# Kernel optimization log

Measured on AMD Instinct MI355X. Metric: run time of the kernel, lower is better.

The kernel has to match this reference:

```python
import jax, jax.numpy as jnp
import numpy as np

N_T, N_Q = 32768, 4096
E_T, E_Q = 1048576, 131072
H = 128
VOCAB = 1001  # num_features + 1
NUM_LAYERS = 3


def _sage_conv(x, edge_index, Wl, bl, Wr):
    # PyG SAGEConv, aggr='mean': out = lin_l(mean_j x_j) + lin_r(x_i)
    src, dst = edge_index[0], edge_index[1]
    n = x.shape[0]
    agg = jax.ops.segment_sum(x[src], dst, num_segments=n)          # [n, H]
    cnt = jax.ops.segment_sum(jnp.ones((src.shape[0],), x.dtype), dst, num_segments=n)
    mean = agg / jnp.maximum(cnt, 1.0)[:, None]
    return mean @ Wl.T + bl + x @ Wr.T


def setup_inputs() -> dict:
    key = jax.random.key(0)
    ks = jax.random.split(key, 12)
    target_x = jax.random.randint(ks[0], (N_T,), 0, VOCAB, dtype=jnp.int64 if jax.config.jax_enable_x64 else jnp.int32)
    query_x = jax.random.randint(ks[1], (N_Q,), 0, VOCAB, dtype=target_x.dtype)
    target_edge_index = jax.random.randint(ks[2], (2, E_T), 0, N_T, dtype=target_x.dtype)
    query_edge_index = jax.random.randint(ks[3], (2, E_Q), 0, N_Q, dtype=target_x.dtype)
    mask = jax.random.bernoulli(ks[4], 0.5, (N_Q, N_T))
    emb = jax.random.normal(ks[5], (VOCAB, H), jnp.float32) * 0.02
    s = 1.0 / np.sqrt(H)
    Wl = jax.random.uniform(ks[6], (NUM_LAYERS, H, H), jnp.float32, -s, s)
    bl = jax.random.uniform(ks[7], (NUM_LAYERS, H), jnp.float32, -s, s)
    Wr = jax.random.uniform(ks[8], (NUM_LAYERS, H, H), jnp.float32, -s, s)
    return {"target_x": target_x, "query_x": query_x,
            "target_edge_index": target_edge_index, "query_edge_index": query_edge_index,
            "mask": mask, "emb": emb, "Wl": Wl, "bl": bl, "Wr": Wr}


def reference(target_x, query_x, target_edge_index, query_edge_index, mask, emb, Wl, bl, Wr):
    et = emb[target_x]  # [N_T, H]
    eq = emb[query_x]   # [N_Q, H]
    for i in range(NUM_LAYERS):
        et = jax.nn.elu(_sage_conv(et, target_edge_index, Wl[i], bl[i], Wr[i]))
        eq = jax.nn.elu(_sage_conv(eq, query_edge_index, Wl[i], bl[i], Wr[i]))
    fmask = mask.astype(jnp.float32)
    att = (eq @ et.T) * fmask / jnp.sqrt(jnp.float32(H)) + (-1e9) * (1.0 - fmask)
    att = jax.nn.softmax(att, axis=1)
    return att[None]  # [1, N_Q, N_T]
```

## Files before the change

### kernel.cpp

```cpp
#include <hip/hip_runtime.h>
#include <stdint.h>

#define N_T 32768
#define N_Q 4096
#define E_T 1048576
#define E_Q 131072
#define H   128
#define NL  3
#define VOCAB 1001

typedef float    f32x4 __attribute__((ext_vector_type(4)));
typedef int      i32x4 __attribute__((ext_vector_type(4)));
typedef unsigned u32x4 __attribute__((ext_vector_type(4)));
typedef _Float16 f16x8 __attribute__((ext_vector_type(8)));

__device__ __forceinline__ ushort f2h(float x){
  union{_Float16 h; ushort u;} c; c.h = (_Float16)x; return c.u;
}
__device__ __forceinline__ float h2f(unsigned u){
  union{ushort u; _Float16 h;} c; c.u = (ushort)u; return (float)c.h;
}

__global__ void zero_i32_k(int* p, int n){
  int i = blockIdx.x*blockDim.x + threadIdx.x;
  if(i<n) p[i]=0;
}
__global__ void zero_f32_k(float* p, int n){
  int i = blockIdx.x*blockDim.x + threadIdx.x;
  if(i<n) p[i]=0.f;
}

__global__ void detect_mask_k(const unsigned* m, int* flag){
  int t = threadIdx.x;
  int f = 0;
  for(int j=t;j<4096;j+=256){
    unsigned v = m[j];
    if(v > 1u) f |= (v & 0xFEFEFEFEu) ? 2 : 1;
  }
  if(f) atomicOr(flag, f);
}

__global__ void wcvt_k(const float* __restrict__ Wl, const float* __restrict__ Wr,
                       ushort* __restrict__ WH, ushort* __restrict__ WLo){
  int i = blockIdx.x*blockDim.x + threadIdx.x;
  if(i >= NL*128*64) return;
  int k  = (i & 63) * 4;
  int c  = (i >> 6) & 127;
  int l  = i >> 13;
  const float* src = (k < 128)
      ? &Wl[((size_t)l*128 + c)*128 + k]
      : &Wr[((size_t)l*128 + c)*128 + (k-128)];
  float4 v = *(const float4*)src;
  ushort4 h, lo;
  h.x = f2h(v.x); lo.x = f2h(v.x - h2f(h.x));
  h.y = f2h(v.y); lo.y = f2h(v.y - h2f(h.y));
  h.z = f2h(v.z); lo.z = f2h(v.z - h2f(h.z));
  h.w = f2h(v.w); lo.w = f2h(v.w - h2f(h.w));
  size_t off = ((size_t)l*128 + c)*256 + k;
  *(ushort4*)&WH[off]  = h;
  *(ushort4*)&WLo[off] = lo;
}

__global__ void ecvt_k(const float* __restrict__ e, ushort* __restrict__ o){
  int i = blockIdx.x*blockDim.x + threadIdx.x;
  if(i >= VOCAB*H/8) return;
  float4 v0 = ((const float4*)e)[(size_t)i*2];
  float4 v1 = ((const float4*)e)[(size_t)i*2 + 1];
  uint4 u;
  u.x = (unsigned)f2h(v0.x) | ((unsigned)f2h(v0.y)<<16);
  u.y = (unsigned)f2h(v0.z) | ((unsigned)f2h(v0.w)<<16);
  u.z = (unsigned)f2h(v1.x) | ((unsigned)f2h(v1.y)<<16);
  u.w = (unsigned)f2h(v1.z) | ((unsigned)f2h(v1.w)<<16);
  ((uint4*)o)[i] = u;
}

__global__ void count_k(const int* __restrict__ dst, int E, int* cnt){
  int i = blockIdx.x*blockDim.x + threadIdx.x;
  if(i<E) atomicAdd(&cnt[dst[i]], 1);
}

__global__ void scan_k(const int* __restrict__ cnt, int n, int* rp, int* pos){
  __shared__ int part[1024];
  int t = threadIdx.x;
  int chunk = (n + 1023) >> 10;
  int lo = t*chunk, hi = lo+chunk; if(hi>n) hi=n;
  int s = 0;
  for(int i=lo;i<hi;i++) s += cnt[i];
  part[t] = s;
  __syncthreads();
  for(int off=1; off<1024; off<<=1){
    int v = (t >= off) ? part[t-off] : 0;
    __syncthreads();
    part[t] += v;
    __syncthreads();
  }
  int run = (t==0) ? 0 : part[t-1];
  for(int i=lo;i<hi;i++){ rp[i]=run; pos[i]=run; run += cnt[i]; }
  if(t==0) rp[n] = part[1023];
}

__global__ void fill_k(const int* __restrict__ src, const int* __restrict__ dst,
                       int E, int* pos, int* csr){
  int i = blockIdx.x*blockDim.x + threadIdx.x;
  if(i<E){
    int p = atomicAdd(&pos[dst[i]], 1);
    csr[p] = src[i];
  }
}

__global__ void agg_k(const ushort* __restrict__ x, const int* __restrict__ nid,
                      const ushort* __restrict__ emb16,
                      const int* __restrict__ rp, const int* __restrict__ csr,
                      ushort* __restrict__ agg, int N){
  int wid = (int)(((size_t)blockIdx.x*blockDim.x + threadIdx.x) >> 6);
  int lane = threadIdx.x & 63;
  if(wid >= N) return;
  const unsigned* xw = (const unsigned*)x;
  const unsigned* ew = (const unsigned*)emb16;
  int rs = rp[wid], re = rp[wid+1];
  float px[8], py[8];
  #pragma unroll
  for(int q=0;q<8;q++){ px[q]=0.f; py[q]=0.f; }
  int j = rs;
  if(nid){
    for(; j+8 <= re; j+=8){
      #pragma unroll
      for(int q=0;q<8;q++){
        unsigned u = ew[(size_t)nid[csr[j+q]]*64 + lane];
        px[q] += h2f(u & 0xFFFFu); py[q] += h2f(u >> 16);
      }
    }
    for(; j < re; j++){
      unsigned u = ew[(size_t)nid[csr[j]]*64 + lane];
      px[0] += h2f(u & 0xFFFFu); py[0] += h2f(u >> 16);
    }
  } else {
    for(; j+8 <= re; j+=8){
      #pragma unroll
      for(int q=0;q<8;q++){
        unsigned u = xw[(size_t)csr[j+q]*64 + lane];
        px[q] += h2f(u & 0xFFFFu); py[q] += h2f(u >> 16);
      }
    }
    for(; j < re; j++){
      unsigned u = xw[(size_t)csr[j]*64 + lane];
      px[0] += h2f(u & 0xFFFFu); py[0] += h2f(u >> 16);
    }
  }
  float sx = ((px[0]+px[1]) + (px[2]+px[3])) + ((px[4]+px[5]) + (px[6]+px[7]));
  float sy = ((py[0]+py[1]) + (py[2]+py[3])) + ((py[4]+py[5]) + (py[6]+py[7]));
  int c = re - rs; if(c < 1) c = 1;
  float inv = 1.0f / (float)c;
  ((unsigned*)agg)[(size_t)wid*64 + lane] =
      (unsigned)f2h(sx*inv) | ((unsigned)f2h(sy*inv) << 16);
}

__global__ __launch_bounds__(256,3) void layer_k(
    const ushort* __restrict__ agg, const ushort* __restrict__ xprev,
    const int* __restrict__ nid, const ushort* __restrict__ emb16,
    const ushort* __restrict__ WH, const ushort* __restrict__ WLo,
    const float* __restrict__ bl, ushort* __restrict__ out16){
  __shared__ ushort SM3[3*128*64];
  ushort* SA = SM3;
  ushort* SH = SM3 + 8192;
  ushort* SL = SM3 + 16384;
  int t = threadIdx.x;
  int r0g = blockIdx.x * 128;
  int lane = t & 63;
  int w = t >> 6;
  int wr = w >> 1, wc = w & 1;
  int fr = lane & 15, kg0 = lane >> 4;
  f32x4 acc[4][4] = {};
  for(int kt=0; kt<4; kt++){
    __syncthreads();
    int ko = (kt & 1) * 64;
    #pragma unroll
    for(int it=0; it<4; it++){
      int idx = t + it*256;
      int row = idx >> 3, k8 = idx & 7;
      int sw = (k8 ^ (row & 7)) * 8;
      uint4 av;
      if(kt < 2){
        av = *(const uint4*)&agg[(size_t)(r0g+row)*H + ko + k8*8];
      } else if(nid){
        av = *(const uint4*)&emb16[(size_t)nid[r0g+row]*H + ko + k8*8];
      } else {
        av = *(const uint4*)&xprev[(size_t)(r0g+row)*H + ko + k8*8];
      }
      *(uint4*)&SA[row*64 + sw] = av;
      *(uint4*)&SH[row*64 + sw] = *(const uint4*)&WH[row*256 + kt*64 + k8*8];
      *(uint4*)&SL[row*64 + sw] = *(const uint4*)&WLo[row*256 + kt*64 + k8*8];
    }
    __syncthreads();
    #pragma unroll
    for(int s=0; s<2; s++){
      int kg = s*4 + kg0;
      f16x8 a[4], bh[4], blo[4];
      #pragma unroll
      for(int m=0;m<4;m++){
        int ar = wr*64 + m*16 + fr;
        a[m] = *(const f16x8*)&SA[ar*64 + ((kg ^ (ar & 7)) << 3)];
      }
      #pragma unroll
      for(int n=0;n<4;n++){
        int bc = wc*64 + n*16 + fr;
        int ib = bc*64 + ((kg ^ (bc & 7)) << 3);
        bh[n]  = *(const f16x8*)&SH[ib];
        blo[n] = *(const f16x8*)&SL[ib];
      }
      #pragma unroll
      for(int m=0;m<4;m++)
        #pragma unroll
        for(int n=0;n<4;n++){
          acc[m][n] = __builtin_amdgcn_mfma_f32_16x16x32_f16(a[m], bh[n],  acc[m][n], 0,0,0);
          acc[m][n] = __builtin_amdgcn_mfma_f32_16x16x32_f16(a[m], blo[n], acc[m][n], 0,0,0);
        }
    }
  }
  __syncthreads();
  ushort* LT = SM3;
  #pragma unroll
  for(int n=0;n<4;n++){
    int c = wc*64 + n*16 + fr;
    float b = bl[c];
    #pragma unroll
    for(int m=0;m<4;m++){
      int r = wr*64 + m*16 + kg0*4;
      #pragma unroll
      for(int reg=0;reg<4;reg++){
        float v = acc[m][n][reg] + b;
        v = (v > 0.f) ? v : expm1f(v);
        LT[(r+reg)*128 + c] = f2h(v);
      }
    }
  }
  __syncthreads();
  #pragma unroll
  for(int i=0;i<8;i++){
    int idx = t + i*256;
    int row = idx >> 4, c8 = idx & 15;
    *(uint4*)&out16[(size_t)(r0g+row)*H + c8*8] = *(uint4*)&LT[row*128 + c8*8];
  }
}

__device__ __forceinline__ unsigned nib8(unsigned x, unsigned y){
  unsigned r = (x & 0xFu) | ((x>>4)&0xF0u) | ((x>>8)&0xF00u) | ((x>>12)&0xF000u);
  unsigned s = (y & 0xFu) | ((y>>4)&0xF0u) | ((y>>8)&0xF00u) | ((y>>12)&0xF000u);
  return r | (s<<16);
}
__device__ __forceinline__ unsigned pk4(unsigned u){
  return ((u & 0xFFu)       ? 1u : 0u) | ((u & 0xFF00u)     ? 2u : 0u)
       | ((u & 0xFF0000u)   ? 4u : 0u) | ((u & 0xFF000000u) ? 8u : 0u);
}

__device__ __forceinline__ void stage_mask_tile(const void* maskp, int mb,
    int gr0, int gc0, unsigned* MB, uint8_t* NB, unsigned* bitsOut, int t){
  if(mb & 2){
    const f32x4* base = (const f32x4*)maskp;
    #pragma unroll
    for(int i=0;i<16;i++){
      int idx = i*256 + t;
      int row = idx >> 5, c4 = idx & 31;
      f32x4 v = __builtin_nontemporal_load(
          &base[((size_t)(gr0+row)*N_T + gc0) / 4 + c4]);
      NB[row*32 + c4] = (uint8_t)((unsigned)(v[0]!=0.f) | ((unsigned)(v[1]!=0.f)<<1)
                                | ((unsigned)(v[2]!=0.f)<<2) | ((unsigned)(v[3]!=0.f)<<3));
    }
  } else if(mb & 1){
    const uint8_t* base = (const uint8_t*)maskp;
    #pragma unroll
    for(int i=0;i<16;i++){
      int idx = i*256 + t;
      int row = idx >> 5, c4 = idx & 31;
      unsigned u = __builtin_nontemporal_load(
          (const unsigned*)&base[(size_t)(gr0+row)*N_T + gc0 + c4*4]);
      NB[row*32 + c4] = (uint8_t)pk4(u);
    }
  } else {
    const i32x4* base = (const i32x4*)maskp;
    #pragma unroll
    for(int i=0;i<16;i++){
      int idx = i*256 + t;
      int row = idx >> 5, c4 = idx & 31;
      i32x4 v = __builtin_nontemporal_load(
          &base[((size_t)(gr0+row)*N_T + gc0) / 4 + c4]);
      NB[row*32 + c4] = (uint8_t)((unsigned)(v[0]!=0) | ((unsigned)(v[1]!=0)<<1)
                                | ((unsigned)(v[2]!=0)<<2) | ((unsigned)(v[3]!=0)<<3));
    }
  }
  __syncthreads();
  if(t < 128){
    uint4 a = *(const uint4*)&NB[t*32];
    uint4 b = *(const uint4*)&NB[t*32 + 16];
    unsigned w0 = nib8(a.x, a.y), w1 = nib8(a.z, a.w);
    unsigned w2 = nib8(b.x, b.y), w3 = nib8(b.z, b.w);
    MB[t*4]   = w0; MB[t*4+1] = w1;
    MB[t*4+2] = w2; MB[t*4+3] = w3;
    if(bitsOut){
      uint4 o; o.x=w0; o.y=w1; o.z=w2; o.w=w3;
      *(uint4*)&bitsOut[(size_t)(gr0 + t)*(N_T/32) + (gc0 >> 5)] = o;
    }
  }
}

__device__ __forceinline__ void qk_gemm(
    const ushort* __restrict__ A16, const ushort* __restrict__ B16,
    int abase, int bbase, int t, ushort* SM, f32x4 (&acc)[4][4]){
  ushort* AB = SM;
  ushort* BB = SM + 8192;
  int lane = t & 63;
  int w = t >> 6;
  int wr = w >> 1, wc = w & 1;
  int fr = lane & 15, kg0 = lane >> 4;
  for(int kt=0; kt<2; kt++){
    __syncthreads();
    #pragma unroll
    for(int it=0; it<4; it++){
      int idx = t + it*256;
      int row = idx >> 3, k8 = idx & 7;
      int sw = (k8 ^ (row & 7)) * 8;
      *(uint4*)&AB[row*64 + sw] = *(const uint4*)&A16[(size_t)(abase+row)*H + kt*64 + k8*8];
      *(uint4*)&BB[row*64 + sw] = *(const uint4*)&B16[(size_t)(bbase+row)*H + kt*64 + k8*8];
    }
    __syncthreads();
    #pragma unroll
    for(int s=0; s<2; s++){
      int kg = s*4 + kg0;
      f16x8 a[4], b[4];
      #pragma unroll
      for(int m=0;m<4;m++){
        int ar = wr*64 + m*16 + fr;
        a[m] = *(const f16x8*)&AB[ar*64 + ((kg ^ (ar & 7)) << 3)];
      }
      #pragma unroll
      for(int n=0;n<4;n++){
        int bc = wc*64 + n*16 + fr;
        b[n] = *(const f16x8*)&BB[bc*64 + ((kg ^ (bc & 7)) << 3)];
      }
      #pragma unroll
      for(int m=0;m<4;m++)
        #pragma unroll
        for(int n=0;n<4;n++)
          acc[m][n] = __builtin_amdgcn_mfma_f32_16x16x32_f16(a[m], b[n], acc[m][n], 0,0,0);
    }
  }
}

__global__ __launch_bounds__(256,4) void attsum_k(
    const ushort* __restrict__ eq16, const ushort* __restrict__ et16,
    const void* __restrict__ maskp, const int* __restrict__ flag,
    unsigned* __restrict__ bitsOut, float* __restrict__ rowsum){
  __shared__ ushort SM[2*128*64];
  __shared__ __align__(16) unsigned MB[512];
  __shared__ float RS[128][2];
  int t = threadIdx.x;
  int gc0 = blockIdx.x * 128;
  int gr0 = blockIdx.y * 128;
  int lane = t & 63;
  int w = t >> 6;
  int wr = w >> 1, wc = w & 1;
  int fr = lane & 15, kg0 = lane >> 4;

  int mb = *flag;
  stage_mask_tile(maskp, mb, gr0, gc0, MB, (uint8_t*)SM, bitsOut, t);

  f32x4 acc[4][4] = {};
  qk_gemm(et16, eq16, gc0, gr0, t, SM, acc);

  const float sc = 0.08838834764831845f;
  #pragma unroll
  for(int n=0;n<4;n++){
    int q = wc*64 + n*16 + fr;
    float s = 0.f;
    #pragma unroll
    for(int m=0;m<4;m++){
      unsigned wb = MB[q*4 + wr*2 + (m>>1)];
      int off = ((m&1)<<4) | (kg0<<2);
      s += ((wb>>(off+0))&1u) ? __expf(acc[m][n][0]*sc) : 0.f;
      s += ((wb>>(off+1))&1u) ? __expf(acc[m][n][1]*sc) : 0.f;
      s += ((wb>>(off+2))&1u) ? __expf(acc[m][n][2]*sc) : 0.f;
      s += ((wb>>(off+3))&1u) ? __expf(acc[m][n][3]*sc) : 0.f;
    }
    s += __shfl_xor(s, 16);
    s += __shfl_xor(s, 32);
    if(lane < 16) RS[q][wr] = s;
  }
  __syncthreads();
  if(t < 128) atomicAdd(&rowsum[gr0 + t], RS[t][0] + RS[t][1]);
}

__global__ __launch_bounds__(256,4) void attout_k(
    const ushort* __restrict__ eq16, const ushort* __restrict__ et16,
    const void* __restrict__ maskp, const int* __restrict__ flag,
    const unsigned* __restrict__ bitsIn, const float* __restrict__ rowsum,
    float* __restrict__ out){
  __shared__ ushort SM[2*128*64];
  __shared__ __align__(16) unsigned MB[512];
  __shared__ float IRS[128];
  int t = threadIdx.x;
  int gc0 = blockIdx.x * 128;
  int gr0 = blockIdx.y * 128;
  int lane = t & 63;
  int w = t >> 6;
  int wr = w >> 1, wc = w & 1;
  int fr = lane & 15, kg0 = lane >> 4;

  if(bitsIn){
    if(t < 128)
      *(uint4*)&MB[t*4] = *(const uint4*)&bitsIn[(size_t)(gr0 + t)*(N_T/32) + (gc0 >> 5)];
  } else {
    int mb = *flag;
    stage_mask_tile(maskp, mb, gr0, gc0, MB, (uint8_t*)SM, nullptr, t);
  }
  if(t < 128) IRS[t] = 1.0f / rowsum[gr0 + t];

  f32x4 acc[4][4] = {};
  qk_gemm(et16, eq16, gc0, gr0, t, SM, acc);

  const float sc = 0.08838834764831845f;
  #pragma unroll
  for(int n=0;n<4;n++){
    int q = wc*64 + n*16 + fr;
    float ir = IRS[q];
    size_t rb = (size_t)(gr0 + q)*N_T + gc0 + wr*64;
    #pragma unroll
    for(int m=0;m<4;m++){
      unsigned wb = MB[q*4 + wr*2 + (m>>1)];
      int off = ((m&1)<<4) | (kg0<<2);
      f32x4 o;
      o[0] = ((wb>>(off+0))&1u) ? __expf(acc[m][n][0]*sc)*ir : 0.f;
      o[1] = ((wb>>(off+1))&1u) ? __expf(acc[m][n][1]*sc)*ir : 0.f;
      o[2] = ((wb>>(off+2))&1u) ? __expf(acc[m][n][2]*sc)*ir : 0.f;
      o[3] = ((wb>>(off+3))&1u) ? __expf(acc[m][n][3]*sc)*ir : 0.f;
      __builtin_nontemporal_store(o, (f32x4*)&out[rb + m*16 + (kg0<<2)]);
    }
  }
}

extern "C" void kernel_launch(void* const* d_in, const int* in_sizes, int n_in,
                              void* d_out, int out_size, void* d_ws, size_t ws_size,
                              hipStream_t stream){
  const int* tx  = (const int*)d_in[0];
  const int* qx  = (const int*)d_in[1];
  const int* te  = (const int*)d_in[2];
  const int* qe  = (const int*)d_in[3];
  const void* mask = d_in[4];
  const float* emb = (const float*)d_in[5];
  const float* Wl  = (const float*)d_in[6];
  const float* bl  = (const float*)d_in[7];
  const float* Wr  = (const float*)d_in[8];
  float* out = (float*)d_out;

  ushort* et16 = (ushort*)d_ws;
  ushort* eq16 = et16 + (size_t)N_T*H;
  float* rowsum = (float*)((char*)d_ws + ((size_t)9 << 20));
  int*   flag   = (int*)(rowsum + N_Q);
  ushort* WH  = (ushort*)((char*)d_ws + ((size_t)10 << 20));
  ushort* WLo = WH + (size_t)NL*128*256;
  ushort* emb16 = (ushort*)((char*)d_ws + ((size_t)11 << 20));
  bool useBits = ws_size >= ((size_t)37 << 20);
  unsigned* bits = useBits ? (unsigned*)((char*)d_ws + ((size_t)19 << 20)) : nullptr;

  char* S = (char*)d_out;
  ushort* xt0  = (ushort*)(S);
  ushort* xt1  = (ushort*)(S + 8388608);
  ushort* aggt = (ushort*)(S + 16777216);
  ushort* xq0  = (ushort*)(S + 25165824);
  ushort* xq1  = (ushort*)(S + 26214400);
  ushort* aggq = (ushort*)(S + 27262976);
  int*   cnt_t = (int*)(S + 28311552);
  int*   rp_t  = cnt_t + N_T;
  int*   pos_t = rp_t + N_T + 1;
  int*   csr_t = pos_t + N_T;
  int*   cnt_q = csr_t + E_T;
  int*   rp_q  = cnt_q + N_Q;
  int*   pos_q = rp_q + N_Q + 1;
  int*   csr_q = pos_q + N_Q;

  zero_i32_k<<<(N_T+255)/256,256,0,stream>>>(cnt_t, N_T);
  zero_i32_k<<<(N_Q+255)/256,256,0,stream>>>(cnt_q, N_Q);
  zero_f32_k<<<(N_Q+255)/256,256,0,stream>>>(rowsum, N_Q);
  zero_i32_k<<<1,256,0,stream>>>(flag, 1);
  detect_mask_k<<<1,256,0,stream>>>((const unsigned*)mask, flag);
  wcvt_k<<<96,256,0,stream>>>(Wl, Wr, WH, WLo);
  ecvt_k<<<(VOCAB*H/8+255)/256,256,0,stream>>>(emb, emb16);

  count_k<<<E_T/256,256,0,stream>>>(te+E_T, E_T, cnt_t);
  scan_k<<<1,1024,0,stream>>>(cnt_t, N_T, rp_t, pos_t);
  fill_k<<<E_T/256,256,0,stream>>>(te, te+E_T, E_T, pos_t, csr_t);
  count_k<<<E_Q/256,256,0,stream>>>(qe+E_Q, E_Q, cnt_q);
  scan_k<<<1,1024,0,stream>>>(cnt_q, N_Q, rp_q, pos_q);
  fill_k<<<E_Q/256,256,0,stream>>>(qe, qe+E_Q, E_Q, pos_q, csr_q);

  ushort* outs_t[NL] = {xt0, xt1, et16};
  ushort* outs_q[NL] = {xq0, xq1, eq16};
  const ushort* cur_t = nullptr;
  const ushort* cur_q = nullptr;
  for(int l=0;l<NL;l++){
    const ushort* wh = WH  + (size_t)l*128*256;
    const ushort* wl = WLo + (size_t)l*128*256;
    const int* nidt = (l==0) ? tx : nullptr;
    const int* nidq = (l==0) ? qx : nullptr;
    agg_k<<<N_T/4,256,0,stream>>>(cur_t, nidt, emb16, rp_t, csr_t, aggt, N_T);
    layer_k<<<N_T/128,256,0,stream>>>(aggt, cur_t, nidt, emb16, wh, wl,
                                      bl+(size_t)l*H, outs_t[l]);
    agg_k<<<N_Q/4,256,0,stream>>>(cur_q, nidq, emb16, rp_q, csr_q, aggq, N_Q);
    layer_k<<<N_Q/128,256,0,stream>>>(aggq, cur_q, nidq, emb16, wh, wl,
                                      bl+(size_t)l*H, outs_q[l]);
    cur_t = outs_t[l];
    cur_q = outs_q[l];
  }

  attsum_k<<<dim3(N_T/128, N_Q/128),256,0,stream>>>(eq16, et16, mask, flag, bits, rowsum);
  attout_k<<<dim3(N_T/128, N_Q/128),256,0,stream>>>(eq16, et16, mask, flag, bits, rowsum, out);
}
```

Before: 711.1 us.

## Merge target/query kernels into combined launches and remap attention tiles per XCD

Fuses the many small setup kernels (zeroing, mask detection, weight/embedding conversion) and pairs each target and query kernel (count, scan, fill, aggregation, layer GEMM) into single launches that split the work by block index. This cuts launch count and lets the small query-side work overlap with the target-side work instead of running serially. The attention kernels move to a 1D grid whose block-to-tile mapping groups column tiles by XCD (bid&7), aiming to improve L2 reuse of et16 within each XCD. The risks are extra branching and mixed block types inside one launch.

```diff
diff --git a/kernel.cpp b/kernel.cpp
--- a/kernel.cpp
+++ b/kernel.cpp
@@ -11,7 +11,6 @@
 
 typedef float    f32x4 __attribute__((ext_vector_type(4)));
 typedef int      i32x4 __attribute__((ext_vector_type(4)));
-typedef unsigned u32x4 __attribute__((ext_vector_type(4)));
 typedef _Float16 f16x8 __attribute__((ext_vector_type(8)));
 
 __device__ __forceinline__ ushort f2h(float x){
@@ -21,65 +20,72 @@
   union{ushort u; _Float16 h;} c; c.u = (ushort)u; return (float)c.h;
 }
 
-__global__ void zero_i32_k(int* p, int n){
-  int i = blockIdx.x*blockDim.x + threadIdx.x;
-  if(i<n) p[i]=0;
-}
-__global__ void zero_f32_k(float* p, int n){
-  int i = blockIdx.x*blockDim.x + threadIdx.x;
-  if(i<n) p[i]=0.f;
-}
-
-__global__ void detect_mask_k(const unsigned* m, int* flag){
-  int t = threadIdx.x;
-  int f = 0;
-  for(int j=t;j<4096;j+=256){
-    unsigned v = m[j];
-    if(v > 1u) f |= (v & 0xFEFEFEFEu) ? 2 : 1;
-  }
-  if(f) atomicOr(flag, f);
-}
-
-__global__ void wcvt_k(const float* __restrict__ Wl, const float* __restrict__ Wr,
-                       ushort* __restrict__ WH, ushort* __restrict__ WLo){
-  int i = blockIdx.x*blockDim.x + threadIdx.x;
-  if(i >= NL*128*64) return;
-  int k  = (i & 63) * 4;
-  int c  = (i >> 6) & 127;
-  int l  = i >> 13;
-  const float* src = (k < 128)
-      ? &Wl[((size_t)l*128 + c)*128 + k]
-      : &Wr[((size_t)l*128 + c)*128 + (k-128)];
-  float4 v = *(const float4*)src;
-  ushort4 h, lo;
-  h.x = f2h(v.x); lo.x = f2h(v.x - h2f(h.x));
-  h.y = f2h(v.y); lo.y = f2h(v.y - h2f(h.y));
-  h.z = f2h(v.z); lo.z = f2h(v.z - h2f(h.z));
-  h.w = f2h(v.w); lo.w = f2h(v.w - h2f(h.w));
-  size_t off = ((size_t)l*128 + c)*256 + k;
-  *(ushort4*)&WH[off]  = h;
-  *(ushort4*)&WLo[off] = lo;
-}
-
-__global__ void ecvt_k(const float* __restrict__ e, ushort* __restrict__ o){
-  int i = blockIdx.x*blockDim.x + threadIdx.x;
-  if(i >= VOCAB*H/8) return;
-  float4 v0 = ((const float4*)e)[(size_t)i*2];
-  float4 v1 = ((const float4*)e)[(size_t)i*2 + 1];
-  uint4 u;
-  u.x = (unsigned)f2h(v0.x) | ((unsigned)f2h(v0.y)<<16);
-  u.y = (unsigned)f2h(v0.z) | ((unsigned)f2h(v0.w)<<16);
-  u.z = (unsigned)f2h(v1.x) | ((unsigned)f2h(v1.y)<<16);
-  u.w = (unsigned)f2h(v1.z) | ((unsigned)f2h(v1.w)<<16);
-  ((uint4*)o)[i] = u;
-}
-
-__global__ void count_k(const int* __restrict__ dst, int E, int* cnt){
-  int i = blockIdx.x*blockDim.x + threadIdx.x;
-  if(i<E) atomicAdd(&cnt[dst[i]], 1);
-}
-
-__global__ void scan_k(const int* __restrict__ cnt, int n, int* rp, int* pos){
+__global__ void setup_k(int* cnt_t, int* cnt_q, float* rowsum, int* flag,
+                        const unsigned* m){
+  int b = blockIdx.x, t = threadIdx.x;
+  if(b < 128){ cnt_t[b*256+t] = 0; }
+  else if(b < 144){ cnt_q[(b-128)*256+t] = 0; }
+  else if(b < 160){ rowsum[(b-144)*256+t] = 0.f; }
+  else {
+    if(t == 0) *flag = 0;
+    __syncthreads();
+    int f = 0;
+    for(int j=t;j<4096;j+=256){
+      unsigned v = m[j];
+      if(v > 1u) f |= (v & 0xFEFEFEFEu) ? 2 : 1;
+    }
+    if(f) atomicOr(flag, f);
+  }
+}
+
+__global__ void cvt_k(const float* __restrict__ Wl, const float* __restrict__ Wr,
+                      ushort* __restrict__ WH, ushort* __restrict__ WLo,
+                      const float* __restrict__ emb, ushort* __restrict__ emb16){
+  int b = blockIdx.x, t = threadIdx.x;
+  if(b < 96){
+    int i = b*256 + t;
+    int k  = (i & 63) * 4;
+    int c  = (i >> 6) & 127;
+    int l  = i >> 13;
+    const float* src = (k < 128)
+        ? &Wl[((size_t)l*128 + c)*128 + k]
+        : &Wr[((size_t)l*128 + c)*128 + (k-128)];
+    float4 v = *(const float4*)src;
+    ushort4 h, lo;
+    h.x = f2h(v.x); lo.x = f2h(v.x - h2f(h.x));
+    h.y = f2h(v.y); lo.y = f2h(v.y - h2f(h.y));
+    h.z = f2h(v.z); lo.z = f2h(v.z - h2f(h.z));
+    h.w = f2h(v.w); lo.w = f2h(v.w - h2f(h.w));
+    size_t off = ((size_t)l*128 + c)*256 + k;
+    *(ushort4*)&WH[off]  = h;
+    *(ushort4*)&WLo[off] = lo;
+  } else {
+    int i = (b-96)*256 + t;
+    if(i >= VOCAB*H/8) return;
+    float4 v0 = ((const float4*)emb)[(size_t)i*2];
+    float4 v1 = ((const float4*)emb)[(size_t)i*2 + 1];
+    uint4 u;
+    u.x = (unsigned)f2h(v0.x) | ((unsigned)f2h(v0.y)<<16);
+    u.y = (unsigned)f2h(v0.z) | ((unsigned)f2h(v0.w)<<16);
+    u.z = (unsigned)f2h(v1.x) | ((unsigned)f2h(v1.y)<<16);
+    u.w = (unsigned)f2h(v1.z) | ((unsigned)f2h(v1.w)<<16);
+    ((uint4*)emb16)[i] = u;
+  }
+}
+
+__global__ void count2_k(const int* __restrict__ te, const int* __restrict__ qe,
+                         int* cnt_t, int* cnt_q){
+  int b = blockIdx.x;
+  if(b < E_T/256){
+    int i = b*256 + threadIdx.x;
+    atomicAdd(&cnt_t[te[E_T + i]], 1);
+  } else {
+    int i = (b - E_T/256)*256 + threadIdx.x;
+    atomicAdd(&cnt_q[qe[E_Q + i]], 1);
+  }
+}
+
+__device__ __forceinline__ void scan_body(const int* cnt, int n, int* rp, int* pos){
   __shared__ int part[1024];
   int t = threadIdx.x;
   int chunk = (n + 1023) >> 10;
@@ -99,22 +105,29 @@
   if(t==0) rp[n] = part[1023];
 }
 
-__global__ void fill_k(const int* __restrict__ src, const int* __restrict__ dst,
-                       int E, int* pos, int* csr){
-  int i = blockIdx.x*blockDim.x + threadIdx.x;
-  if(i<E){
-    int p = atomicAdd(&pos[dst[i]], 1);
-    csr[p] = src[i];
-  }
-}
-
-__global__ void agg_k(const ushort* __restrict__ x, const int* __restrict__ nid,
-                      const ushort* __restrict__ emb16,
-                      const int* __restrict__ rp, const int* __restrict__ csr,
-                      ushort* __restrict__ agg, int N){
-  int wid = (int)(((size_t)blockIdx.x*blockDim.x + threadIdx.x) >> 6);
-  int lane = threadIdx.x & 63;
-  if(wid >= N) return;
+__global__ void scan2_k(const int* cnt_t, int* rp_t, int* pos_t,
+                        const int* cnt_q, int* rp_q, int* pos_q){
+  if(blockIdx.x == 0) scan_body(cnt_t, N_T, rp_t, pos_t);
+  else                scan_body(cnt_q, N_Q, rp_q, pos_q);
+}
+
+__global__ void fill2_k(const int* __restrict__ te, const int* __restrict__ qe,
+                        int* pos_t, int* csr_t, int* pos_q, int* csr_q){
+  int b = blockIdx.x;
+  if(b < E_T/256){
+    int i = b*256 + threadIdx.x;
+    int p = atomicAdd(&pos_t[te[E_T + i]], 1);
+    csr_t[p] = te[i];
+  } else {
+    int i = (b - E_T/256)*256 + threadIdx.x;
+    int p = atomicAdd(&pos_q[qe[E_Q + i]], 1);
+    csr_q[p] = qe[i];
+  }
+}
+
+__device__ __forceinline__ void agg_body(const ushort* x, const int* nid,
+    const ushort* emb16, const int* rp, const int* csr, ushort* agg,
+    int wid, int lane){
   const unsigned* xw = (const unsigned*)x;
   const unsigned* ew = (const unsigned*)emb16;
   int rs = rp[wid], re = rp[wid+1];
@@ -155,17 +168,40 @@
       (unsigned)f2h(sx*inv) | ((unsigned)f2h(sy*inv) << 16);
 }
 
-__global__ __launch_bounds__(256,3) void layer_k(
-    const ushort* __restrict__ agg, const ushort* __restrict__ xprev,
-    const int* __restrict__ nid, const ushort* __restrict__ emb16,
+__global__ void agg2_k(const ushort* xt, const ushort* xq,
+                       const int* nidt, const int* nidq, const ushort* emb16,
+                       const int* rp_t, const int* csr_t,
+                       const int* rp_q, const int* csr_q,
+                       ushort* aggt, ushort* aggq){
+  int b = blockIdx.x;
+  int lane = threadIdx.x & 63;
+  int wv = threadIdx.x >> 6;
+  if(b < N_T/4){
+    agg_body(xt, nidt, emb16, rp_t, csr_t, aggt, b*4 + wv, lane);
+  } else {
+    agg_body(xq, nidq, emb16, rp_q, csr_q, aggq, (b - N_T/4)*4 + wv, lane);
+  }
+}
+
+__global__ __launch_bounds__(256,3) void layer2_k(
+    const ushort* __restrict__ aggT, const ushort* __restrict__ xT,
+    const int* __restrict__ nidT, ushort* __restrict__ outT,
+    const ushort* __restrict__ aggQ, const ushort* __restrict__ xQ,
+    const int* __restrict__ nidQ, ushort* __restrict__ outQ,
+    const ushort* __restrict__ emb16,
     const ushort* __restrict__ WH, const ushort* __restrict__ WLo,
-    const float* __restrict__ bl, ushort* __restrict__ out16){
+    const float* __restrict__ bl){
   __shared__ ushort SM3[3*128*64];
   ushort* SA = SM3;
   ushort* SH = SM3 + 8192;
   ushort* SL = SM3 + 16384;
+  int bq = (int)blockIdx.x - (N_T/128);
+  const ushort* agg   = (bq < 0) ? aggT : aggQ;
+  const ushort* xprev = (bq < 0) ? xT   : xQ;
+  const int*    nid   = (bq < 0) ? nidT : nidQ;
+  ushort*       out16 = (bq < 0) ? outT : outQ;
+  int r0g = ((bq < 0) ? (int)blockIdx.x : bq) * 128;
   int t = threadIdx.x;
-  int r0g = blockIdx.x * 128;
   int lane = t & 63;
   int w = t >> 6;
   int wr = w >> 1, wc = w & 1;
@@ -303,6 +339,13 @@
   }
 }
 
+__device__ __forceinline__ void att_tile(int bid, int& gc0, int& gr0){
+  int xcd = bid & 7;
+  int idx = bid >> 3;
+  gc0 = (xcd*32 + (idx & 31)) * 128;
+  gr0 = (idx >> 5) * 128;
+}
+
 __device__ __forceinline__ void qk_gemm(
     const ushort* __restrict__ A16, const ushort* __restrict__ B16,
     int abase, int bbase, int t, ushort* SM, f32x4 (&acc)[4][4]){
@@ -354,8 +397,8 @@
   __shared__ __align__(16) unsigned MB[512];
   __shared__ float RS[128][2];
   int t = threadIdx.x;
-  int gc0 = blockIdx.x * 128;
-  int gr0 = blockIdx.y * 128;
+  int gc0, gr0;
+  att_tile(blockIdx.x, gc0, gr0);
   int lane = t & 63;
   int w = t >> 6;
   int wr = w >> 1, wc = w & 1;
@@ -398,8 +441,8 @@
   __shared__ __align__(16) unsigned MB[512];
   __shared__ float IRS[128];
   int t = threadIdx.x;
-  int gc0 = blockIdx.x * 128;
-  int gr0 = blockIdx.y * 128;
+  int gc0, gr0;
+  att_tile(blockIdx.x, gc0, gr0);
   int lane = t & 63;
   int w = t >> 6;
   int wr = w >> 1, wc = w & 1;
@@ -477,20 +520,11 @@
   int*   pos_q = rp_q + N_Q + 1;
   int*   csr_q = pos_q + N_Q;
 
-  zero_i32_k<<<(N_T+255)/256,256,0,stream>>>(cnt_t, N_T);
-  zero_i32_k<<<(N_Q+255)/256,256,0,stream>>>(cnt_q, N_Q);
-  zero_f32_k<<<(N_Q+255)/256,256,0,stream>>>(rowsum, N_Q);
-  zero_i32_k<<<1,256,0,stream>>>(flag, 1);
-  detect_mask_k<<<1,256,0,stream>>>((const unsigned*)mask, flag);
-  wcvt_k<<<96,256,0,stream>>>(Wl, Wr, WH, WLo);
-  ecvt_k<<<(VOCAB*H/8+255)/256,256,0,stream>>>(emb, emb16);
-
-  count_k<<<E_T/256,256,0,stream>>>(te+E_T, E_T, cnt_t);
-  scan_k<<<1,1024,0,stream>>>(cnt_t, N_T, rp_t, pos_t);
-  fill_k<<<E_T/256,256,0,stream>>>(te, te+E_T, E_T, pos_t, csr_t);
-  count_k<<<E_Q/256,256,0,stream>>>(qe+E_Q, E_Q, cnt_q);
-  scan_k<<<1,1024,0,stream>>>(cnt_q, N_Q, rp_q, pos_q);
-  fill_k<<<E_Q/256,256,0,stream>>>(qe, qe+E_Q, E_Q, pos_q, csr_q);
+  setup_k<<<161,256,0,stream>>>(cnt_t, cnt_q, rowsum, flag, (const unsigned*)mask);
+  cvt_k<<<159,256,0,stream>>>(Wl, Wr, WH, WLo, emb, emb16);
+  count2_k<<<E_T/256 + E_Q/256,256,0,stream>>>(te, qe, cnt_t, cnt_q);
+  scan2_k<<<2,1024,0,stream>>>(cnt_t, rp_t, pos_t, cnt_q, rp_q, pos_q);
+  fill2_k<<<E_T/256 + E_Q/256,256,0,stream>>>(te, qe, pos_t, csr_t, pos_q, csr_q);
 
   ushort* outs_t[NL] = {xt0, xt1, et16};
   ushort* outs_q[NL] = {xq0, xq1, eq16};
@@ -501,16 +535,15 @@
     const ushort* wl = WLo + (size_t)l*128*256;
     const int* nidt = (l==0) ? tx : nullptr;
     const int* nidq = (l==0) ? qx : nullptr;
-    agg_k<<<N_T/4,256,0,stream>>>(cur_t, nidt, emb16, rp_t, csr_t, aggt, N_T);
-    layer_k<<<N_T/128,256,0,stream>>>(aggt, cur_t, nidt, emb16, wh, wl,
-                                      bl+(size_t)l*H, outs_t[l]);
-    agg_k<<<N_Q/4,256,0,stream>>>(cur_q, nidq, emb16, rp_q, csr_q, aggq, N_Q);
-    layer_k<<<N_Q/128,256,0,stream>>>(aggq, cur_q, nidq, emb16, wh, wl,
-                                      bl+(size_t)l*H, outs_q[l]);
+    agg2_k<<<N_T/4 + N_Q/4,256,0,stream>>>(cur_t, cur_q, nidt, nidq, emb16,
+                                           rp_t, csr_t, rp_q, csr_q, aggt, aggq);
+    layer2_k<<<N_T/128 + N_Q/128,256,0,stream>>>(aggt, cur_t, nidt, outs_t[l],
+                                                 aggq, cur_q, nidq, outs_q[l],
+                                                 emb16, wh, wl, bl+(size_t)l*H);
     cur_t = outs_t[l];
     cur_q = outs_q[l];
   }
 
-  attsum_k<<<dim3(N_T/128, N_Q/128),256,0,stream>>>(eq16, et16, mask, flag, bits, rowsum);
-  attout_k<<<dim3(N_T/128, N_Q/128),256,0,stream>>>(eq16, et16, mask, flag, bits, rowsum, out);
-}
+  attsum_k<<<8192,256,0,stream>>>(eq16, et16, mask, flag, bits, rowsum);
+  attout_k<<<8192,256,0,stream>>>(eq16, et16, mask, flag, bits, rowsum, out);
+}
```

After: 645.5 us. 1.1x faster.
